# Optimization experiments

Hardware: AMD Instinct MI355X
Metric: run time of the kernel (lower is better)

## Reference

```python
import jax, jax.numpy as jnp
import numpy as np

DT = 0.01
B = 2097152
STATE_DIM, LATENT_DIM, INPUT_DIM = 3, 4, 3
TOTAL = STATE_DIM + LATENT_DIM  # 7
HID_L, HID_B = 64, 32


def setup_inputs() -> dict:
    key = jax.random.key(0)
    ks = jax.random.split(key, 16)
    def w(k, shape, fan_in):
        return (jax.random.normal(k, shape, dtype=jnp.float32) / np.sqrt(fan_in)).astype(jnp.float32)
    return {
        "state": jax.random.normal(ks[0], (B, TOTAL), dtype=jnp.float32),
        "u": jax.random.normal(ks[1], (B, INPUT_DIM), dtype=jnp.float32),
        # linear physics prior: s_dot = s@A.T + u@Bm.T ; y_phys = s@C.T
        "A": w(ks[2], (STATE_DIM, STATE_DIM), STATE_DIM),
        "Bm": w(ks[3], (STATE_DIM, INPUT_DIM), INPUT_DIM),
        "C": w(ks[4], (STATE_DIM, STATE_DIM), STATE_DIM),
        # z_gate: Linear(10 -> 7) + sigmoid
        "Wz": w(ks[5], (TOTAL, TOTAL + INPUT_DIM), TOTAL + INPUT_DIM),
        "bz": jnp.full((TOTAL,), 2.0, dtype=jnp.float32),
        # latent_dyn: Linear(10 -> 64) tanh Linear(64 -> 4)
        "W1": w(ks[6], (HID_L, TOTAL + INPUT_DIM), TOTAL + INPUT_DIM),
        "b1": jnp.zeros((HID_L,), dtype=jnp.float32),
        "W2": w(ks[7], (LATENT_DIM, HID_L), HID_L),
        "b2": jnp.zeros((LATENT_DIM,), dtype=jnp.float32),
        # 3 branches stacked: Linear(6 -> 32) tanh Linear(32 -> 1)
        "Wb1": w(ks[8], (3, HID_B, STATE_DIM + INPUT_DIM), STATE_DIM + INPUT_DIM),
        "bb1": jnp.zeros((3, HID_B), dtype=jnp.float32),
        "Wb2": w(ks[9], (3, HID_B), HID_B),
        "bb2": jnp.zeros((3,), dtype=jnp.float32),
    }


def reference(state, u, A, Bm, C, Wz, bz, W1, b1, W2, b2, Wb1, bb1, Wb2, bb2):
    s = state[:, :STATE_DIM]          # [B,3]
    latent = state[:, STATE_DIM:]     # [B,4]
    # physics prior
    s_dot_phys = s @ A.T + u @ Bm.T   # [B,3]
    y_phys = s @ C.T                  # [B,3]
    s_phys_next = s + DT * s_dot_phys
    su = jnp.concatenate([state, u], axis=1)  # [B,10]
    # latent dynamics
    latent_dot = jnp.tanh(su @ W1.T + b1) @ W2.T + b2   # [B,4]
    latent_next = latent + DT * latent_dot
    candidate = jnp.concatenate([s_phys_next, latent_next], axis=1)  # [B,7]
    # update gate
    z = jax.nn.sigmoid(su @ Wz.T + bz)                  # [B,7]
    next_state = z * candidate + (1.0 - z) * state
    # residual branch heads (vectorized over the 3 heads)
    branch_in = jnp.concatenate([s, u], axis=1)         # [B,6]
    h = jnp.tanh(jnp.einsum('bi,khi->bkh', branch_in, Wb1) + bb1)  # [B,3,32]
    residuals = jnp.einsum('bkh,kh->bk', h, Wb2) + bb2  # [B,3]
    y = y_phys + residuals
    return (next_state, y)
```

## Files before the change

kernel.cpp:

```cpp
#include <hip/hip_runtime.h>
#include <stdint.h>


#define DT_C 0.01f
#define NROWS 2097152
#define LOG2E 1.4426950408889634f
#define S2L   2.8853901617779268f

typedef __fp16 h2 __attribute__((ext_vector_type(2)));

__device__ __forceinline__ h2 pkrtz(float a, float b) {
    return __builtin_amdgcn_cvt_pkrtz(a, b);
}

#if __has_builtin(__builtin_amdgcn_fdot2)
__device__ __forceinline__ float fdot2(h2 a, h2 b, float c) {
    return __builtin_amdgcn_fdot2(a, b, c, false);
}
#else
__device__ __forceinline__ float fdot2(h2 a, h2 b, float c) {
    return fmaf((float)a[0], (float)b[0], fmaf((float)a[1], (float)b[1], c));
}
#endif

__device__ __forceinline__ float tanh_pre(float xs) {
    float e = __builtin_amdgcn_exp2f(xs);
    return fmaf(-2.0f, __builtin_amdgcn_rcpf(1.0f + e), 1.0f);
}
__device__ __forceinline__ float sigmoid_pre(float xs) {
    float e = __builtin_amdgcn_exp2f(xs);
    return __builtin_amdgcn_rcpf(1.0f + e);
}

#define W1P_OFF   0
#define WZP_OFF   320
#define WB1P_OFF  355
#define W2P_OFF   643
#define PHYSP_OFF 771
#define CP_OFF    780
#define B1S_OFF   786
#define BZS_OFF   850
#define BB1S_OFF  857

__device__ __forceinline__ uint32_t pack2(float a, float b) {
    h2 v = pkrtz(a, b);
    uint32_t u; __builtin_memcpy(&u, &v, 4); return u;
}

__global__ void prep_kernel(const float* __restrict__ A, const float* __restrict__ Bm,
                            const float* __restrict__ C, const float* __restrict__ Wz,
                            const float* __restrict__ bz, const float* __restrict__ W1,
                            const float* __restrict__ b1, const float* __restrict__ Wb1,
                            const float* __restrict__ bb1, const float* __restrict__ W2,
                            uint32_t* __restrict__ ws)
{
    const int tid = blockIdx.x * blockDim.x + threadIdx.x;
    const int nt = gridDim.x * blockDim.x;
    float* wsf = (float*)ws;

    for (int i = tid; i < 320; i += nt) {
        int h = i / 5, j = i % 5;
        ws[W1P_OFF + i] = pack2(W1[h*10 + 2*j] * S2L, W1[h*10 + 2*j + 1] * S2L);
    }
    for (int i = tid; i < 35; i += nt) {
        int r = i / 5, j = i % 5;
        ws[WZP_OFF + i] = pack2(Wz[r*10 + 2*j] * -LOG2E, Wz[r*10 + 2*j + 1] * -LOG2E);
    }
    for (int i = tid; i < 288; i += nt) {
        int row = i / 3, j = i % 3;
        ws[WB1P_OFF + i] = pack2(Wb1[row*6 + 2*j] * S2L, Wb1[row*6 + 2*j + 1] * S2L);
    }
    for (int i = tid; i < 128; i += nt) {
        int k = i / 32, j = i % 32;
        ws[W2P_OFF + i] = pack2(W2[k*64 + 2*j], W2[k*64 + 2*j + 1]);
    }
    for (int i = tid; i < 9; i += nt) {
        int r = i / 3, j = i % 3;
        float a, b;
        if (j == 0) { a = A[r*3+0];  b = A[r*3+1];  }
        else if (j == 1) { a = A[r*3+2];  b = Bm[r*3+0]; }
        else { a = Bm[r*3+1]; b = Bm[r*3+2]; }
        ws[PHYSP_OFF + i] = pack2(a, b);
    }
    for (int i = tid; i < 6; i += nt) {
        int r = i / 2, j = i % 2;
        float a = (j == 0) ? C[r*3+0] : C[r*3+2];
        float b = (j == 0) ? C[r*3+1] : 0.0f;
        ws[CP_OFF + i] = pack2(a, b);
    }
    for (int i = tid; i < 64; i += nt) wsf[B1S_OFF + i] = b1[i] * S2L;
    for (int i = tid; i < 7;  i += nt) wsf[BZS_OFF + i] = bz[i] * -LOG2E;
    for (int i = tid; i < 96; i += nt) wsf[BB1S_OFF + i] = bb1[i] * S2L;
}

__global__ __launch_bounds__(256) void phygru_kernel(
    const float* __restrict__ state, const float* __restrict__ u,
    const uint32_t* __restrict__ ws, const float* __restrict__ b2,
    const float* __restrict__ Wb2,   const float* __restrict__ bb2,
    float* __restrict__ out)
{
    const int row = blockIdx.x * blockDim.x + threadIdx.x;

    const h2* W1p  = (const h2*)(ws + W1P_OFF);
    const h2* Wzp  = (const h2*)(ws + WZP_OFF);
    const h2* Wb1p = (const h2*)(ws + WB1P_OFF);
    const h2* W2p  = (const h2*)(ws + W2P_OFF);
    const h2* Pp   = (const h2*)(ws + PHYSP_OFF);
    const h2* Cp   = (const h2*)(ws + CP_OFF);
    const float* wsf  = (const float*)ws;
    const float* b1s  = wsf + B1S_OFF;
    const float* bzs  = wsf + BZS_OFF;
    const float* bb1s = wsf + BB1S_OFF;

    float st[7];
    #pragma unroll
    for (int i = 0; i < 7; ++i) st[i] = state[row * 7 + i];
    float uu[3];
    #pragma unroll
    for (int i = 0; i < 3; ++i) uu[i] = u[row * 3 + i];

    h2 suh[5];
    suh[0] = pkrtz(st[0], st[1]);
    suh[1] = pkrtz(st[2], st[3]);
    suh[2] = pkrtz(st[4], st[5]);
    suh[3] = pkrtz(st[6], uu[0]);
    suh[4] = pkrtz(uu[1], uu[2]);
    h2 bih[3];
    bih[0] = suh[0];
    bih[1] = pkrtz(st[2], uu[0]);
    bih[2] = suh[4];

    float sp[3], yp[3];
    #pragma unroll
    for (int r = 0; r < 3; ++r) {
        float sd = fdot2(Pp[r*3+0], bih[0],
                   fdot2(Pp[r*3+1], bih[1],
                   fdot2(Pp[r*3+2], bih[2], 0.0f)));
        sp[r] = fmaf(DT_C, sd, st[r]);
        yp[r] = fdot2(Cp[r*2+0], bih[0], fdot2(Cp[r*2+1], bih[1], 0.0f));
    }

    float ld0 = b2[0], ld1 = b2[1], ld2 = b2[2], ld3 = b2[3];
    #pragma unroll
    for (int hp = 0; hp < 32; ++hp) {
        const int h0 = 2 * hp, h1 = 2 * hp + 1;
        float a0 = b1s[h0], a1 = b1s[h1];
        #pragma unroll
        for (int j = 0; j < 5; ++j) {
            a0 = fdot2(W1p[h0*5 + j], suh[j], a0);
            a1 = fdot2(W1p[h1*5 + j], suh[j], a1);
        }
        h2 th = pkrtz(tanh_pre(a0), tanh_pre(a1));
        ld0 = fdot2(W2p[0*32 + hp], th, ld0);
        ld1 = fdot2(W2p[1*32 + hp], th, ld1);
        ld2 = fdot2(W2p[2*32 + hp], th, ld2);
        ld3 = fdot2(W2p[3*32 + hp], th, ld3);
    }
    float ln[4];
    ln[0] = fmaf(DT_C, ld0, st[3]);
    ln[1] = fmaf(DT_C, ld1, st[4]);
    ln[2] = fmaf(DT_C, ld2, st[5]);
    ln[3] = fmaf(DT_C, ld3, st[6]);

    float ns[7];
    #pragma unroll
    for (int j = 0; j < 7; ++j) {
        float a = bzs[j];
        #pragma unroll
        for (int i = 0; i < 5; ++i) a = fdot2(Wzp[j*5 + i], suh[i], a);
        float z = sigmoid_pre(a);
        float cand = (j < 3) ? sp[j] : ln[j - 3];
        ns[j] = fmaf(z, cand - st[j], st[j]);
    }

    float res[3];
    #pragma unroll
    for (int k = 0; k < 3; ++k) {
        float r = bb2[k];
        #pragma unroll
        for (int h = 0; h < 32; ++h) {
            float a = bb1s[k*32 + h];
            #pragma unroll
            for (int j = 0; j < 3; ++j)
                a = fdot2(Wb1p[(k*32 + h)*3 + j], bih[j], a);
            r = fmaf(Wb2[k*32 + h], tanh_pre(a), r);
        }
        res[k] = r;
    }

    #pragma unroll
    for (int j = 0; j < 7; ++j) out[row * 7 + j] = ns[j];
    float* yout = out + (size_t)NROWS * 7;
    #pragma unroll
    for (int k = 0; k < 3; ++k) yout[row * 3 + k] = yp[k] + res[k];
}

extern "C" void kernel_launch(void* const* d_in, const int* in_sizes, int n_in,
                              void* d_out, int out_size, void* d_ws, size_t ws_size,
                              hipStream_t stream) {
    const float* state = (const float*)d_in[0];
    const float* u     = (const float*)d_in[1];
    const float* A     = (const float*)d_in[2];
    const float* Bm    = (const float*)d_in[3];
    const float* C     = (const float*)d_in[4];
    const float* Wz    = (const float*)d_in[5];
    const float* bz    = (const float*)d_in[6];
    const float* W1    = (const float*)d_in[7];
    const float* b1    = (const float*)d_in[8];
    const float* W2    = (const float*)d_in[9];
    const float* b2    = (const float*)d_in[10];
    const float* Wb1   = (const float*)d_in[11];
    const float* bb1   = (const float*)d_in[12];
    const float* Wb2   = (const float*)d_in[13];
    const float* bb2   = (const float*)d_in[14];
    float* out = (float*)d_out;
    uint32_t* ws = (uint32_t*)d_ws;

    prep_kernel<<<4, 256, 0, stream>>>(A, Bm, C, Wz, bz, W1, b1, Wb1, bb1, W2, ws);
    phygru_kernel<<<NROWS / 256, 256, 0, stream>>>(state, u, ws, b2, Wb2, bb2, out);
}
```

Before: 259.7 us.

## Replace exp/rcp tanh and sigmoid with shared-memory linear-interpolation LUT

Builds a 512-entry tanh table (value plus slope) in LDS at the start of every block and evaluates all tanh and sigmoid activations by clamping, splitting into integer and fractional parts, and interpolating from it. The prep kernel now folds the table scale and offset into the weights and biases, and sigmoid is written as 0.5*tanh(x/2)+0.5. The aim is to replace the transcendental exp2 and rcp instructions with cheaper ALU work plus an LDS gather. In exchange, every block recomputes the table and synchronises, there is a random-access LDS load per activation that can hit bank conflicts, and accuracy drops to piecewise-linear with outputs clamped beyond roughly ±8.

```diff
diff --git a/kernel.cpp b/kernel.cpp
--- a/kernel.cpp
+++ b/kernel.cpp
@@ -2,10 +2,14 @@
 #include <stdint.h>
 
 
-#define DT_C 0.01f
+#define DT_C  0.01f
 #define NROWS 2097152
 #define LOG2E 1.4426950408889634f
-#define S2L   2.8853901617779268f
+#define TBL_H   0.03125f
+#define INV_H   32.0f
+#define INV_H2  16.0f
+#define TBL_C   256.0f
+#define TBL_MAX 511.999f
 
 typedef __fp16 h2 __attribute__((ext_vector_type(2)));
 
@@ -23,13 +27,33 @@
 }
 #endif
 
-__device__ __forceinline__ float tanh_pre(float xs) {
-    float e = __builtin_amdgcn_exp2f(xs);
-    return fmaf(-2.0f, __builtin_amdgcn_rcpf(1.0f + e), 1.0f);
-}
-__device__ __forceinline__ float sigmoid_pre(float xs) {
-    float e = __builtin_amdgcn_exp2f(xs);
-    return __builtin_amdgcn_rcpf(1.0f + e);
+__device__ __forceinline__ float tanh_ref(float x) {
+    float e = __builtin_amdgcn_exp2f(x * (2.0f * LOG2E));
+    return 1.0f - 2.0f * __builtin_amdgcn_rcpf(1.0f + e);
+}
+
+__device__ __forceinline__ float fract_f(float x) {
+#if __has_builtin(__builtin_amdgcn_fractf)
+    return __builtin_amdgcn_fractf(x);
+#else
+    return x - truncf(x);
+#endif
+}
+
+__device__ __forceinline__ float med3f(float x, float lo, float hi) {
+#if __has_builtin(__builtin_amdgcn_fmed3f)
+    return __builtin_amdgcn_fmed3f(x, lo, hi);
+#else
+    return fminf(fmaxf(x, lo), hi);
+#endif
+}
+
+__device__ __forceinline__ float tanh_lut(float t, const float2* lut) {
+    float tc = med3f(t, 0.0f, TBL_MAX);
+    float fr = fract_f(tc);
+    int   i  = (int)tc;
+    float2 e = lut[i];
+    return fmaf(e.y, fr, e.x);
 }
 
 #define W1P_OFF   0
@@ -60,15 +84,15 @@
 
     for (int i = tid; i < 320; i += nt) {
         int h = i / 5, j = i % 5;
-        ws[W1P_OFF + i] = pack2(W1[h*10 + 2*j] * S2L, W1[h*10 + 2*j + 1] * S2L);
+        ws[W1P_OFF + i] = pack2(W1[h*10 + 2*j] * INV_H, W1[h*10 + 2*j + 1] * INV_H);
     }
     for (int i = tid; i < 35; i += nt) {
         int r = i / 5, j = i % 5;
-        ws[WZP_OFF + i] = pack2(Wz[r*10 + 2*j] * -LOG2E, Wz[r*10 + 2*j + 1] * -LOG2E);
+        ws[WZP_OFF + i] = pack2(Wz[r*10 + 2*j] * INV_H2, Wz[r*10 + 2*j + 1] * INV_H2);
     }
     for (int i = tid; i < 288; i += nt) {
         int row = i / 3, j = i % 3;
-        ws[WB1P_OFF + i] = pack2(Wb1[row*6 + 2*j] * S2L, Wb1[row*6 + 2*j + 1] * S2L);
+        ws[WB1P_OFF + i] = pack2(Wb1[row*6 + 2*j] * INV_H, Wb1[row*6 + 2*j + 1] * INV_H);
     }
     for (int i = tid; i < 128; i += nt) {
         int k = i / 32, j = i % 32;
@@ -88,9 +112,9 @@
         float b = (j == 0) ? C[r*3+1] : 0.0f;
         ws[CP_OFF + i] = pack2(a, b);
     }
-    for (int i = tid; i < 64; i += nt) wsf[B1S_OFF + i] = b1[i] * S2L;
-    for (int i = tid; i < 7;  i += nt) wsf[BZS_OFF + i] = bz[i] * -LOG2E;
-    for (int i = tid; i < 96; i += nt) wsf[BB1S_OFF + i] = bb1[i] * S2L;
+    for (int i = tid; i < 64; i += nt) wsf[B1S_OFF + i] = fmaf(b1[i], INV_H, TBL_C);
+    for (int i = tid; i < 7;  i += nt) wsf[BZS_OFF + i] = fmaf(bz[i], INV_H2, TBL_C);
+    for (int i = tid; i < 96; i += nt) wsf[BB1S_OFF + i] = fmaf(bb1[i], INV_H, TBL_C);
 }
 
 __global__ __launch_bounds__(256) void phygru_kernel(
@@ -99,6 +123,20 @@
     const float* __restrict__ Wb2,   const float* __restrict__ bb2,
     float* __restrict__ out)
 {
+    __shared__ float2 lut[512];
+    {
+        const int t0 = threadIdx.x;
+        #pragma unroll
+        for (int r = 0; r < 2; ++r) {
+            int j = t0 + r * 256;
+            float x  = (j - 256) * TBL_H;
+            float v0 = tanh_ref(x);
+            float v1 = tanh_ref(x + TBL_H);
+            lut[j] = make_float2(v0, v1 - v0);
+        }
+    }
+    __syncthreads();
+
     const int row = blockIdx.x * blockDim.x + threadIdx.x;
 
     const h2* W1p  = (const h2*)(ws + W1P_OFF);
@@ -150,7 +188,7 @@
             a0 = fdot2(W1p[h0*5 + j], suh[j], a0);
             a1 = fdot2(W1p[h1*5 + j], suh[j], a1);
         }
-        h2 th = pkrtz(tanh_pre(a0), tanh_pre(a1));
+        h2 th = pkrtz(tanh_lut(a0, lut), tanh_lut(a1, lut));
         ld0 = fdot2(W2p[0*32 + hp], th, ld0);
         ld1 = fdot2(W2p[1*32 + hp], th, ld1);
         ld2 = fdot2(W2p[2*32 + hp], th, ld2);
@@ -168,7 +206,7 @@
         float a = bzs[j];
         #pragma unroll
         for (int i = 0; i < 5; ++i) a = fdot2(Wzp[j*5 + i], suh[i], a);
-        float z = sigmoid_pre(a);
+        float z = fmaf(0.5f, tanh_lut(a, lut), 0.5f);
         float cand = (j < 3) ? sp[j] : ln[j - 3];
         ns[j] = fmaf(z, cand - st[j], st[j]);
     }
@@ -183,7 +221,7 @@
             #pragma unroll
             for (int j = 0; j < 3; ++j)
                 a = fdot2(Wb1p[(k*32 + h)*3 + j], bih[j], a);
-            r = fmaf(Wb2[k*32 + h], tanh_pre(a), r);
+            r = fmaf(Wb2[k*32 + h], tanh_lut(a, lut), r);
         }
         res[k] = r;
     }
```

New measurement: 250.1 us. 3.7% less time.
